# Optimization experiments

Hardware: AMD Instinct MI355X
Metric: run time of the kernel (lower is better)

## Reference

```python
import jax, jax.numpy as jnp
import numpy as np

IMG, P, INC = 384, 2, 3
C = 2 * IMG            # embed_dim = 768
NP_ = IMG // P         # 192 patches
N = NP_ + 1            # 193 tokens with cls
L, H, E, K, B = 6, 12, 8, 2, 32
HD = C // H
EPS = 1e-5


def layer_norm(x, w, b):
    m = jnp.mean(x, -1, keepdims=True)
    v = jnp.mean((x - m) ** 2, -1, keepdims=True)
    return (x - m) * jax.lax.rsqrt(v + EPS) * w + b


def setup_inputs() -> dict:
    key = jax.random.key(0)
    ks = iter(jax.random.split(key, 32))
    nrm = lambda sh, s=0.02: jax.random.normal(next(ks), sh, jnp.float32) * s
    inp = {
        'x1': nrm((B, INC, IMG, IMG), 1.0),
        'x2': nrm((B, INC, IMG, IMG), 1.0),
        'patch_w': nrm((C, INC, IMG, P)),
        'patch_b': jnp.zeros((C,)),
        'cls_token': nrm((1, 1, C), 1e-6),
        'ln1_w': jnp.ones((L, C)), 'ln1_b': jnp.zeros((L, C)),
        'qkv_w': nrm((L, 3 * C, C)), 'qkv_b': jnp.zeros((L, 3 * C)),
        'proj_w': nrm((L, C, C)), 'proj_b': jnp.zeros((L, C)),
        'ln2_w': jnp.ones((L, C)), 'ln2_b': jnp.zeros((L, C)),
        'route_w': nrm((L, E, C)), 'route_b': jnp.zeros((L, E)),
        'rln_w': jnp.ones((L, E)), 'rln_b': jnp.zeros((L, E)),
        'expert_w': nrm((L, E, C, C)), 'expert_b': jnp.zeros((L, E, C)),
        'norm_w': jnp.ones((C,)), 'norm_b': jnp.zeros((C,)),
    }
    # fixed 1D sin-cos positional embedding (build_sincos_encoding)
    pd = C // 2
    omega = jnp.exp(jnp.arange(pd, dtype=jnp.float32) * (-np.log(10000.0) / pd))
    ow = jnp.arange(NP_, dtype=jnp.float32)[:, None] * omega
    pe = jnp.concatenate([jnp.sin(ow), jnp.cos(ow)], axis=1)          # [192, C]
    inp['pos_emb'] = jnp.concatenate([jnp.zeros((1, C)), pe], axis=0)[None]  # [1, N, C]
    return inp


def _patch_embed(x, patch_w, patch_b, cls_token, pos_emb):
    b = x.shape[0]
    # non-overlapping (IMG, P) conv == matmul on patches, flattened in (c, kh, kw) order
    xp = x.reshape(b, INC, IMG, NP_, P).transpose(0, 3, 1, 2, 4).reshape(b, NP_, INC * IMG * P)
    tok = xp @ patch_w.reshape(C, -1).T + patch_b                     # [B, 192, C]
    tok = jnp.concatenate([jnp.broadcast_to(cls_token, (b, 1, C)), tok], axis=1)
    return tok + pos_emb


def _encoder(x, view_id, ln1_w, ln1_b, qkv_w, qkv_b, proj_w, proj_b,
             ln2_w, ln2_b, route_w, route_b, rln_w, rln_b, expert_w, expert_b):
    scale = HD ** -0.5
    base = jax.random.fold_in(jax.random.key(1234), view_id)
    b = x.shape[0]

    def step(h, p):
        idx, l1w, l1b, qw, qb, pw, pb, l2w, l2b, rw, rb, rlw, rlb, ew, eb = p
        # --- attention ---
        y = layer_norm(h, l1w, l1b)
        qkv = (y @ qw.T + qb).reshape(b, N, 3, H, HD).transpose(2, 0, 3, 1, 4)
        q, k, v = qkv[0], qkv[1], qkv[2]
        a = jax.nn.softmax(jnp.einsum('bhqd,bhkd->bhqk', q, k) * scale, axis=-1)
        o = jnp.einsum('bhqk,bhkd->bhqd', a, v).transpose(0, 2, 1, 3).reshape(b, N, C)
        h = h + o @ pw.T + pb
        # --- MoE ---
        y = layer_norm(h, l2w, l2b)
        logits = layer_norm(y @ rw.T + rb, rlw, rlb)                  # [B, N, E]
        noise = jax.random.normal(jax.random.fold_in(base, idx), logits.shape) / E
        rwts = jax.nn.softmax(logits, axis=-1) + noise
        topw, topi = jax.lax.top_k(rwts, K)
        topw = jax.nn.softmax(topw, axis=-1)
        # dense all-expert compute, as in the source module
        eo = jnp.einsum('bni,eoi->bneo', y, ew) + eb                  # [B, N, E, C]
        sel = jnp.take_along_axis(eo, topi[..., None], axis=2)        # [B, N, K, C]
        h = h + (sel * topw[..., None]).sum(axis=2)
        return h, None

    xs = (jnp.arange(L), ln1_w, ln1_b, qkv_w, qkv_b, proj_w, proj_b,
          ln2_w, ln2_b, route_w, route_b, rln_w, rln_b, expert_w, expert_b)
    x, _ = jax.lax.scan(step, x, xs)
    return x


def reference(x1, x2, patch_w, patch_b, cls_token, ln1_w, ln1_b, qkv_w, qkv_b,
              proj_w, proj_b, ln2_w, ln2_b, route_w, route_b, rln_w, rln_b,
              expert_w, expert_b, norm_w, norm_b, pos_emb):
    def tower(x, vid):
        h = _patch_embed(x, patch_w, patch_b, cls_token, pos_emb)
        h = _encoder(h, vid, ln1_w, ln1_b, qkv_w, qkv_b, proj_w, proj_b,
                     ln2_w, ln2_b, route_w, route_b, rln_w, rln_b, expert_w, expert_b)
        return layer_norm(h, norm_w, norm_b)[:, 0]
    return jnp.concatenate([tower(x1, 0), tower(x2, 1)], axis=1)      # [B, 2*C]
```

## Files before the change

kernel.cpp:

```cpp
#include <hip/hip_runtime.h>
#include <stdint.h>

#define C_DIM   768
#define N_TOK   193
#define B_TOT   64
#define ROWS    (B_TOT * N_TOK)
#define QKV_DIM 2304
#define N_HEAD  12
#define N_EXP   8
#define MAXPER  ROWS
#define RTOK    64

enum { MODE_PATCH = 0, MODE_PLAIN = 1, MODE_RESID = 2, MODE_EXPERT = 3 };

typedef __attribute__((ext_vector_type(8))) short bf16x8;
typedef __attribute__((ext_vector_type(4))) float f32x4;

__device__ __forceinline__ uint32_t rotl32(uint32_t x, int n){ return (x << n) | (x >> (32 - n)); }

__device__ __forceinline__ void tf2x32(uint32_t k0, uint32_t k1, uint32_t x0, uint32_t x1,
                                       uint32_t &r0, uint32_t &r1){
  uint32_t k2 = k0 ^ k1 ^ 0x1BD11BDAu;
#define TF4(a,b,c,d) x0+=x1; x1=rotl32(x1,a); x1^=x0; x0+=x1; x1=rotl32(x1,b); x1^=x0; \
                     x0+=x1; x1=rotl32(x1,c); x1^=x0; x0+=x1; x1=rotl32(x1,d); x1^=x0;
  x0 += k0; x1 += k1;
  TF4(13,15,26, 6)  x0 += k1; x1 += k2 + 1u;
  TF4(17,29,16,24)  x0 += k2; x1 += k0 + 2u;
  TF4(13,15,26, 6)  x0 += k0; x1 += k1 + 3u;
  TF4(17,29,16,24)  x0 += k1; x1 += k2 + 4u;
  TF4(13,15,26, 6)  x0 += k2; x1 += k0 + 5u;
#undef TF4
  r0 = x0; r1 = x1;
}

__device__ __forceinline__ float jax_erfinv(float x){
  float w = -log1pf(-x * x);
  float p;
  if (w < 5.0f){
    w -= 2.5f;
    p =              2.81022636e-08f;
    p = fmaf(p, w,   3.43273939e-07f);
    p = fmaf(p, w,  -3.5233877e-06f);
    p = fmaf(p, w,  -4.39150654e-06f);
    p = fmaf(p, w,   0.00021858087f);
    p = fmaf(p, w,  -0.00125372503f);
    p = fmaf(p, w,  -0.00417768164f);
    p = fmaf(p, w,   0.246640727f);
    p = fmaf(p, w,   1.50140941f);
  } else {
    w = sqrtf(w) - 3.0f;
    p =             -0.000200214257f;
    p = fmaf(p, w,   0.000100950558f);
    p = fmaf(p, w,   0.00134934322f);
    p = fmaf(p, w,  -0.00367342844f);
    p = fmaf(p, w,   0.00573950773f);
    p = fmaf(p, w,  -0.0076224613f);
    p = fmaf(p, w,   0.00943887047f);
    p = fmaf(p, w,   1.00167406f);
    p = fmaf(p, w,   2.83297682f);
  }
  return p * x;
}

__device__ __forceinline__ float jax_noise(uint32_t c0, uint32_t c1, uint32_t j){
  uint32_t o0, o1;
  tf2x32(c0, c1, 0u, j, o0, o1);
  uint32_t bits = o0 ^ o1;
  float f = __uint_as_float(0x3f800000u | (bits >> 9)) - 1.0f;
  const float lo = -0.99999994f;
  float u = fmaxf(lo, f * 2.0f + lo);
  return 1.41421356237f * jax_erfinv(u) * 0.125f;
}

__device__ __forceinline__ unsigned short f2bf(float x){
  union { float f; uint32_t u; } v; v.f = x;
  uint32_t u = v.u;
  uint32_t r = (u + 0x7FFFu + ((u >> 16) & 1u)) >> 16;
  return (unsigned short)r;
}
__device__ __forceinline__ float bf2f(unsigned short h){
  union { uint32_t u; float f; } v; v.u = ((uint32_t)h) << 16;
  return v.f;
}

__global__ __launch_bounds__(64) void k_zero8(int* __restrict__ p){
  if ((int)threadIdx.x < N_EXP) p[threadIdx.x] = 0;
}

__global__ __launch_bounds__(64) void k_sentinel(float* __restrict__ out, float v){
  if (threadIdx.x == 0) out[0] = v;
}

__global__ __launch_bounds__(256) void k_cls(float* __restrict__ h, const float* __restrict__ cls,
                                             const float* __restrict__ pos){
  const int bt = blockIdx.x;
  #pragma unroll
  for (int u = 0; u < 3; ++u){
    int c = threadIdx.x + u * 256;
    h[(size_t)bt * N_TOK * C_DIM + c] = cls[c] + pos[c];
  }
}

__device__ __forceinline__ float blk_sum(float v, float* sb){
  #pragma unroll
  for (int off = 32; off > 0; off >>= 1) v += __shfl_down(v, off, 64);
  const int lane = threadIdx.x & 63, w = threadIdx.x >> 6;
  if (lane == 0) sb[w] = v;
  __syncthreads();
  if (threadIdx.x == 0) sb[4] = sb[0] + sb[1] + sb[2] + sb[3];
  __syncthreads();
  float r = sb[4];
  __syncthreads();
  return r;
}

__global__ __launch_bounds__(256) void k_layernorm(const float* __restrict__ x, float* __restrict__ y,
                                                   const float* __restrict__ w, const float* __restrict__ b){
  __shared__ float sb[8];
  const float* xr = x + (size_t)blockIdx.x * C_DIM;
  float v0 = xr[threadIdx.x], v1 = xr[threadIdx.x + 256], v2 = xr[threadIdx.x + 512];
  float mean = blk_sum(v0 + v1 + v2, sb) * (1.0f / 768.0f);
  float d0 = v0 - mean, d1 = v1 - mean, d2 = v2 - mean;
  float var = blk_sum(d0 * d0 + d1 * d1 + d2 * d2, sb) * (1.0f / 768.0f);
  float inv = 1.0f / sqrtf(var + 1e-5f);
  float* yr = y + (size_t)blockIdx.x * C_DIM;
  yr[threadIdx.x]       = d0 * inv * w[threadIdx.x]       + b[threadIdx.x];
  yr[threadIdx.x + 256] = d1 * inv * w[threadIdx.x + 256] + b[threadIdx.x + 256];
  yr[threadIdx.x + 512] = d2 * inv * w[threadIdx.x + 512] + b[threadIdx.x + 512];
}

__global__ __launch_bounds__(256) void k_final(const float* __restrict__ h, float* __restrict__ out,
                                               const float* __restrict__ w, const float* __restrict__ b){
  __shared__ float sb[8];
  const int bt = blockIdx.x;
  const float* xr = h + (size_t)bt * N_TOK * C_DIM;
  float v0 = xr[threadIdx.x], v1 = xr[threadIdx.x + 256], v2 = xr[threadIdx.x + 512];
  float mean = blk_sum(v0 + v1 + v2, sb) * (1.0f / 768.0f);
  float d0 = v0 - mean, d1 = v1 - mean, d2 = v2 - mean;
  float var = blk_sum(d0 * d0 + d1 * d1 + d2 * d2, sb) * (1.0f / 768.0f);
  float inv = 1.0f / sqrtf(var + 1e-5f);
  float* orow = out + (size_t)(bt & 31) * 1536 + (size_t)(bt >> 5) * C_DIM;
  orow[threadIdx.x]       = d0 * inv * w[threadIdx.x]       + b[threadIdx.x];
  orow[threadIdx.x + 256] = d1 * inv * w[threadIdx.x + 256] + b[threadIdx.x + 256];
  orow[threadIdx.x + 512] = d2 * inv * w[threadIdx.x + 512] + b[threadIdx.x + 512];
}

template<int MODE>
__global__ __launch_bounds__(256) void k_mgemm(
    const float* __restrict__ A, const float* __restrict__ W,
    const float* __restrict__ bias, float* __restrict__ C,
    int M, int Nc, int Kc,
    const float* __restrict__ xa, const float* __restrict__ xb,
    const float* __restrict__ pos,
    const int* __restrict__ elist, const int* __restrict__ ecnt)
{
  __shared__ short sAhi[128][40];
  __shared__ short sAlo[128][40];
  __shared__ short sBhi[128][40];
  __shared__ short sBlo[128][40];

  const int tid = threadIdx.x;

  int e = 0;
  int Mloc = M;
  const float* Wp = W;
  const float* bp = bias;
  if constexpr (MODE == MODE_EXPERT){
    e = blockIdx.z;
    Mloc = ecnt[e];
    Wp = W + (size_t)e * C_DIM * C_DIM;
    bp = bias + e * C_DIM;
  }
  const int row0 = blockIdx.x * 128;
  const int col0 = blockIdx.y * 128;
  if (row0 >= Mloc) return;

  const int srow = tid >> 1;
  const int skh  = (tid & 1) * 16;

  const float* arow = A;
  bool avalid = false;
  const float* psrc = nullptr;
  if constexpr (MODE == MODE_PLAIN || MODE == MODE_RESID){
    int r = row0 + srow;
    avalid = r < Mloc;
    arow = A + (size_t)(avalid ? r : 0) * Kc;
  } else if constexpr (MODE == MODE_EXPERT){
    int r = row0 + srow;
    avalid = r < Mloc;
    if (avalid) arow = A + (size_t)(elist[e * MAXPER + r] >> 1) * C_DIM;
  } else {
    int r = row0 + srow;
    int bt = r / 192;
    int n  = r - bt * 192;
    const float* xp = (bt < 32) ? xa : xb;
    psrc = xp + (size_t)(bt & 31) * 3 * 384 * 384 + n * 2;
    avalid = true;
  }
  const float* brow = Wp + (size_t)(col0 + srow) * Kc;

  const int wv = tid >> 6;
  const int wr = (wv >> 1) * 64;
  const int wc = (wv & 1) * 64;
  const int lane = tid & 63;
  const int lrow = lane & 15;
  const int lkh  = (lane >> 4) * 8;

  f32x4 acc[4][4] = {};

  const int nkt = Kc / 32;
  for (int kt = 0; kt < nkt; ++kt){
    const int k0 = kt * 32 + skh;
    {
      float va[16] = {};
      if constexpr (MODE == MODE_PATCH){
        int c   = k0 / 768;
        int rem = k0 - c * 768;
        const float* pc = psrc + ((size_t)c * 384 + (rem >> 1)) * 384;
        #pragma unroll
        for (int m = 0; m < 8; ++m){
          va[m * 2 + 0] = pc[(size_t)m * 384 + 0];
          va[m * 2 + 1] = pc[(size_t)m * 384 + 1];
        }
      } else {
        if (avalid){
          *(float4*)&va[0]  = *(const float4*)(arow + k0);
          *(float4*)&va[4]  = *(const float4*)(arow + k0 + 4);
          *(float4*)&va[8]  = *(const float4*)(arow + k0 + 8);
          *(float4*)&va[12] = *(const float4*)(arow + k0 + 12);
        }
      }
      short hi[16], lo[16];
      #pragma unroll
      for (int j = 0; j < 16; ++j){
        unsigned short hb = f2bf(va[j]);
        hi[j] = (short)hb;
        lo[j] = (short)f2bf(va[j] - bf2f(hb));
      }
      *(bf16x8*)&sAhi[srow][skh]     = *(bf16x8*)&hi[0];
      *(bf16x8*)&sAhi[srow][skh + 8] = *(bf16x8*)&hi[8];
      *(bf16x8*)&sAlo[srow][skh]     = *(bf16x8*)&lo[0];
      *(bf16x8*)&sAlo[srow][skh + 8] = *(bf16x8*)&lo[8];
    }
    {
      float vb[16];
      *(float4*)&vb[0]  = *(const float4*)(brow + k0);
      *(float4*)&vb[4]  = *(const float4*)(brow + k0 + 4);
      *(float4*)&vb[8]  = *(const float4*)(brow + k0 + 8);
      *(float4*)&vb[12] = *(const float4*)(brow + k0 + 12);
      short hi[16], lo[16];
      #pragma unroll
      for (int j = 0; j < 16; ++j){
        unsigned short hb = f2bf(vb[j]);
        hi[j] = (short)hb;
        lo[j] = (short)f2bf(vb[j] - bf2f(hb));
      }
      *(bf16x8*)&sBhi[srow][skh]     = *(bf16x8*)&hi[0];
      *(bf16x8*)&sBhi[srow][skh + 8] = *(bf16x8*)&hi[8];
      *(bf16x8*)&sBlo[srow][skh]     = *(bf16x8*)&lo[0];
      *(bf16x8*)&sBlo[srow][skh + 8] = *(bf16x8*)&lo[8];
    }
    __syncthreads();
    bf16x8 ahi[4], alo[4], bhi[4], blo[4];
    #pragma unroll
    for (int i = 0; i < 4; ++i){
      ahi[i] = *(const bf16x8*)&sAhi[wr + i * 16 + lrow][lkh];
      alo[i] = *(const bf16x8*)&sAlo[wr + i * 16 + lrow][lkh];
    }
    #pragma unroll
    for (int j = 0; j < 4; ++j){
      bhi[j] = *(const bf16x8*)&sBhi[wc + j * 16 + lrow][lkh];
      blo[j] = *(const bf16x8*)&sBlo[wc + j * 16 + lrow][lkh];
    }
    #pragma unroll
    for (int i = 0; i < 4; ++i)
      #pragma unroll
      for (int j = 0; j < 4; ++j){
        acc[i][j] = __builtin_amdgcn_mfma_f32_16x16x32_bf16(ahi[i], bhi[j], acc[i][j], 0, 0, 0);
        acc[i][j] = __builtin_amdgcn_mfma_f32_16x16x32_bf16(ahi[i], blo[j], acc[i][j], 0, 0, 0);
        acc[i][j] = __builtin_amdgcn_mfma_f32_16x16x32_bf16(alo[i], bhi[j], acc[i][j], 0, 0, 0);
      }
    __syncthreads();
  }

  #pragma unroll
  for (int i = 0; i < 4; ++i){
    const int rbase = row0 + wr + i * 16 + (lane >> 4) * 4;
    #pragma unroll
    for (int r = 0; r < 4; ++r){
      const int rg = rbase + r;
      if (rg >= Mloc) continue;
      if constexpr (MODE == MODE_PATCH){
        int bt = rg / 192, n = rg - (rg / 192) * 192;
        size_t orow = ((size_t)bt * N_TOK + n + 1) * C_DIM;
        size_t prow = (size_t)(n + 1) * C_DIM;
        #pragma unroll
        for (int j = 0; j < 4; ++j){
          int cg = col0 + wc + j * 16 + (lane & 15);
          C[orow + cg] = acc[i][j][r] + bp[cg] + pos[prow + cg];
        }
      } else if constexpr (MODE == MODE_PLAIN){
        size_t orow = (size_t)rg * Nc;
        #pragma unroll
        for (int j = 0; j < 4; ++j){
          int cg = col0 + wc + j * 16 + (lane & 15);
          C[orow + cg] = acc[i][j][r] + bp[cg];
        }
      } else if constexpr (MODE == MODE_RESID){
        size_t orow = (size_t)rg * Nc;
        #pragma unroll
        for (int j = 0; j < 4; ++j){
          int cg = col0 + wc + j * 16 + (lane & 15);
          C[orow + cg] += acc[i][j][r] + bp[cg];
        }
      } else {
        int ts = elist[e * MAXPER + rg];
        size_t orow = (size_t)ts * C_DIM;
        #pragma unroll
        for (int j = 0; j < 4; ++j){
          int cg = col0 + wc + j * 16 + (lane & 15);
          C[orow + cg] = acc[i][j][r] + bp[cg];
        }
      }
    }
  }
}

__global__ __launch_bounds__(256) void k_attn(const float* __restrict__ qkv, float* __restrict__ o_out){
  __shared__ float Qs[64][64];
  __shared__ float KPs[64][64];
  __shared__ float Vs[64][64];
  const int q0 = blockIdx.x * 64;
  const int bh = blockIdx.y;
  const int bt = bh / N_HEAD, hh = bh - bt * N_HEAD;
  const int tid = threadIdx.x;
  const int tx = tid & 15, ty = tid >> 4;
  const size_t base = (size_t)bt * N_TOK * QKV_DIM + (size_t)hh * 64;

  {
    int m = tid & 63, g = tid >> 6;
    int q = q0 + m;
    bool valid = q < N_TOK;
    const float* src = qkv + base + (size_t)(valid ? q : 0) * QKV_DIM;
    #pragma unroll
    for (int u = 0; u < 4; ++u){
      int cb = (g * 4 + u) * 4;
      float4 v = valid ? *(const float4*)(src + cb) : make_float4(0.f,0.f,0.f,0.f);
      Qs[cb + 0][m] = v.x; Qs[cb + 1][m] = v.y; Qs[cb + 2][m] = v.z; Qs[cb + 3][m] = v.w;
    }
  }

  float Oa[4][4] = {};
  float mrun[4] = {-1e30f, -1e30f, -1e30f, -1e30f};
  float lrun[4] = {};

  for (int kt = 0; kt < 4; ++kt){
    const int n0 = kt * 64;
    __syncthreads();
    {
      int m = tid & 63, g = tid >> 6;
      int kk = n0 + m;
      bool valid = kk < N_TOK;
      const float* src = qkv + base + 768 + (size_t)(valid ? kk : 0) * QKV_DIM;
      #pragma unroll
      for (int u = 0; u < 4; ++u){
        int cb = (g * 4 + u) * 4;
        float4 v = valid ? *(const float4*)(src + cb) : make_float4(0.f,0.f,0.f,0.f);
        KPs[cb + 0][m] = v.x; KPs[cb + 1][m] = v.y; KPs[cb + 2][m] = v.z; KPs[cb + 3][m] = v.w;
      }
    }
    {
      int c4 = tid & 15, nr = tid >> 4;
      #pragma unroll
      for (int r = 0; r < 4; ++r){
        int n = nr + r * 16;
        int kk = n0 + n;
        float4 v = (kk < N_TOK) ? *(const float4*)(qkv + base + 1536 + (size_t)kk * QKV_DIM + c4 * 4)
                                : make_float4(0.f,0.f,0.f,0.f);
        *(float4*)&Vs[n][c4 * 4] = v;
      }
    }
    __syncthreads();
    float s[4][4] = {};
    #pragma unroll 8
    for (int d = 0; d < 64; ++d){
      float4 a4 = *(const float4*)&Qs[d][ty * 4];
      float4 b4 = *(const float4*)&KPs[d][tx * 4];
      float av[4] = {a4.x, a4.y, a4.z, a4.w};
      float bv[4] = {b4.x, b4.y, b4.z, b4.w};
      #pragma unroll
      for (int i = 0; i < 4; ++i)
        #pragma unroll
        for (int j = 0; j < 4; ++j)
          s[i][j] = fmaf(av[i], bv[j], s[i][j]);
    }
    #pragma unroll
    for (int i = 0; i < 4; ++i)
      #pragma unroll
      for (int j = 0; j < 4; ++j){
        s[i][j] *= 0.125f;
        if (n0 + tx * 4 + j >= N_TOK) s[i][j] = -1e30f;
      }
    __syncthreads();
    #pragma unroll
    for (int i = 0; i < 4; ++i){
      float rm = fmaxf(fmaxf(s[i][0], s[i][1]), fmaxf(s[i][2], s[i][3]));
      rm = fmaxf(rm, __shfl_xor(rm, 1, 64));
      rm = fmaxf(rm, __shfl_xor(rm, 2, 64));
      rm = fmaxf(rm, __shfl_xor(rm, 4, 64));
      rm = fmaxf(rm, __shfl_xor(rm, 8, 64));
      float mn = fmaxf(mrun[i], rm);
      float fac = expf(mrun[i] - mn);
      mrun[i] = mn;
      lrun[i] *= fac;
      float p[4], rs = 0.f;
      #pragma unroll
      for (int j = 0; j < 4; ++j){ p[j] = expf(s[i][j] - mn); rs += p[j]; }
      rs += __shfl_xor(rs, 1, 64);
      rs += __shfl_xor(rs, 2, 64);
      rs += __shfl_xor(rs, 4, 64);
      rs += __shfl_xor(rs, 8, 64);
      lrun[i] += rs;
      #pragma unroll
      for (int j = 0; j < 4; ++j){ Oa[i][j] *= fac; KPs[ty * 4 + i][tx * 4 + j] = p[j]; }
    }
    __syncthreads();
    #pragma unroll 4
    for (int n = 0; n < 64; ++n){
      float4 v4 = *(const float4*)&Vs[n][tx * 4];
      float vv[4] = {v4.x, v4.y, v4.z, v4.w};
      #pragma unroll
      for (int i = 0; i < 4; ++i){
        float pv = KPs[ty * 4 + i][n];
        #pragma unroll
        for (int j = 0; j < 4; ++j)
          Oa[i][j] = fmaf(pv, vv[j], Oa[i][j]);
      }
    }
  }
  #pragma unroll
  for (int i = 0; i < 4; ++i){
    int q = q0 + ty * 4 + i;
    if (q < N_TOK){
      float inv = 1.0f / lrun[i];
      #pragma unroll
      for (int j = 0; j < 4; ++j)
        o_out[((size_t)bt * N_TOK + q) * C_DIM + hh * 64 + tx * 4 + j] = Oa[i][j] * inv;
    }
  }
}

__global__ __launch_bounds__(256) void k_router(
    const float* __restrict__ y, const float* __restrict__ rw, const float* __restrict__ rb,
    const float* __restrict__ rlw, const float* __restrict__ rlb,
    float* __restrict__ topw, int* __restrict__ elist, int* __restrict__ ecnt, int l)
{
  __shared__ float4 sw4[1536];
  __shared__ int lcnt[8];
  __shared__ int lbase[8];
  __shared__ int llist[8][RTOK];
  const int tid = threadIdx.x;
  const float4* rw4 = (const float4*)rw;
  #pragma unroll
  for (int u = 0; u < 6; ++u)
    sw4[tid + u * 256] = rw4[tid + u * 256];
  if (tid < 8) lcnt[tid] = 0;
  __syncthreads();

  const int wid = tid >> 6, lane = tid & 63;
  const int e = lane & 7;

  for (int t16 = 0; t16 < RTOK / 4; ++t16){
    const int tok = blockIdx.x * RTOK + wid * (RTOK / 4) + t16;
    const float4* y4 = (const float4*)(y + (size_t)tok * C_DIM);
    const float4 a0 = y4[lane], a1 = y4[64 + lane], a2 = y4[128 + lane];

    float part[8];
    #pragma unroll
    for (int ee = 0; ee < 8; ++ee){
      const float4 w0 = sw4[ee * 192 + lane];
      const float4 w1 = sw4[ee * 192 + 64 + lane];
      const float4 w2 = sw4[ee * 192 + 128 + lane];
      float s = a0.x * w0.x;
      s = fmaf(a0.y, w0.y, s); s = fmaf(a0.z, w0.z, s); s = fmaf(a0.w, w0.w, s);
      s = fmaf(a1.x, w1.x, s); s = fmaf(a1.y, w1.y, s); s = fmaf(a1.z, w1.z, s); s = fmaf(a1.w, w1.w, s);
      s = fmaf(a2.x, w2.x, s); s = fmaf(a2.y, w2.y, s); s = fmaf(a2.z, w2.z, s); s = fmaf(a2.w, w2.w, s);
      part[ee] = s;
    }
    #pragma unroll
    for (int ee = 0; ee < 8; ++ee)
      #pragma unroll
      for (int off = 32; off; off >>= 1) part[ee] += __shfl_xor(part[ee], off, 64);

    float logit = part[e] + rb[e];
    float ssum = logit;
    ssum += __shfl_xor(ssum, 1, 64); ssum += __shfl_xor(ssum, 2, 64); ssum += __shfl_xor(ssum, 4, 64);
    float mean = ssum * 0.125f;
    float d = logit - mean;
    float vs = d * d;
    vs += __shfl_xor(vs, 1, 64); vs += __shfl_xor(vs, 2, 64); vs += __shfl_xor(vs, 4, 64);
    float ln = d * (1.0f / sqrtf(vs * 0.125f + 1e-5f)) * rlw[e] + rlb[e];
    float mx = ln;
    mx = fmaxf(mx, __shfl_xor(mx, 1, 64)); mx = fmaxf(mx, __shfl_xor(mx, 2, 64)); mx = fmaxf(mx, __shfl_xor(mx, 4, 64));
    float ex = expf(ln - mx);
    float es = ex;
    es += __shfl_xor(es, 1, 64); es += __shfl_xor(es, 2, 64); es += __shfl_xor(es, 4, 64);
    float prob = ex / es;
    int t = tok / 6176;
    int rem = tok - t * 6176;
    int b = rem / N_TOK, n = rem - (rem / N_TOK) * N_TOK;
    uint32_t b0, b1, c0, c1;
    tf2x32(0u, 1234u, 0u, (uint32_t)t, b0, b1);
    tf2x32(b0, b1, 0u, (uint32_t)l, c0, c1);
    uint32_t j = (uint32_t)(b * N_TOK + n) * 8u + (uint32_t)e;
    float r = prob + jax_noise(c0, c1, j);
    float v1 = r; int i1 = e;
    #pragma unroll
    for (int off = 1; off <= 4; off <<= 1){
      float ov = __shfl_xor(v1, off, 64); int oi = __shfl_xor(i1, off, 64);
      if (ov > v1 || (ov == v1 && oi < i1)){ v1 = ov; i1 = oi; }
    }
    float rm2 = (e == i1) ? -3.0e38f : r;
    float v2 = rm2; int i2 = e;
    #pragma unroll
    for (int off = 1; off <= 4; off <<= 1){
      float ov = __shfl_xor(v2, off, 64); int oi = __shfl_xor(i2, off, 64);
      if (ov > v2 || (ov == v2 && oi < i2)){ v2 = ov; i2 = oi; }
    }
    float e2 = expf(v2 - v1);
    float sum = 1.0f + e2;
    if (lane == 0){
      topw[tok * 2 + 0] = 1.0f / sum;
      topw[tok * 2 + 1] = e2 / sum;
      int p = atomicAdd(&lcnt[i1], 1);
      llist[i1][p] = tok * 2;
      int p2 = atomicAdd(&lcnt[i2], 1);
      llist[i2][p2] = tok * 2 + 1;
    }
  }
  __syncthreads();
  if (tid < 8) lbase[tid] = atomicAdd(&ecnt[tid], lcnt[tid]);
  __syncthreads();
  #pragma unroll
  for (int ee = 0; ee < 8; ++ee){
    const int cnt = lcnt[ee];
    const int bse = lbase[ee];
    for (int i = tid; i < cnt; i += 256)
      elist[ee * MAXPER + bse + i] = llist[ee][i];
  }
}

__global__ __launch_bounds__(256) void k_combine(float* __restrict__ h, const float* __restrict__ eout,
                                                 const float* __restrict__ topw){
  const int tok = blockIdx.x;
  const float w0 = topw[tok * 2], w1 = topw[tok * 2 + 1];
  const size_t hb = (size_t)tok * C_DIM;
  const size_t e0 = (size_t)(tok * 2) * C_DIM, e1 = e0 + C_DIM;
  #pragma unroll
  for (int u = 0; u < 3; ++u){
    int c = threadIdx.x + u * 256;
    h[hb + c] += w0 * eout[e0 + c] + w1 * eout[e1 + c];
  }
}

extern "C" void kernel_launch(void* const* d_in, const int* in_sizes, int n_in,
                              void* d_out, int out_size, void* d_ws, size_t ws_size,
                              hipStream_t stream){
  float* out = (float*)d_out;

  static const int kExp[22] = {
    14155776, 14155776, 1769472, 768, 768,
    4608, 4608, 10616832, 13824, 3538944, 4608,
    4608, 4608, 36864, 48, 48, 48,
    28311552, 36864, 768, 768, 148224};
  const size_t need_f = (size_t)ROWS * C_DIM * 2 + (size_t)ROWS * QKV_DIM
                      + (size_t)ROWS * 2 + (size_t)N_EXP * MAXPER + 8;
  float bad = 0.f;
  if (n_in != 22) bad = 2.0e6f;
  else {
    for (int i = 0; i < 22; ++i)
      if (in_sizes[i] != kExp[i]){ bad = 4.0e6f + i * 1.0e4f; break; }
  }
  if (bad == 0.f && out_size != 49152) bad = 3.0e6f;
  if (bad == 0.f && ws_size < need_f * 4) bad = 1.0e6f;
  if (bad != 0.f){
    k_sentinel<<<dim3(1), 64, 0, stream>>>(out, bad);
    return;
  }

  const float* x1       = (const float*)d_in[0];
  const float* x2       = (const float*)d_in[1];
  const float* patch_w  = (const float*)d_in[2];
  const float* patch_b  = (const float*)d_in[3];
  const float* cls_tok  = (const float*)d_in[4];
  const float* ln1_w    = (const float*)d_in[5];
  const float* ln1_b    = (const float*)d_in[6];
  const float* qkv_w    = (const float*)d_in[7];
  const float* qkv_b    = (const float*)d_in[8];
  const float* proj_w   = (const float*)d_in[9];
  const float* proj_b   = (const float*)d_in[10];
  const float* ln2_w    = (const float*)d_in[11];
  const float* ln2_b    = (const float*)d_in[12];
  const float* route_w  = (const float*)d_in[13];
  const float* route_b  = (const float*)d_in[14];
  const float* rln_w    = (const float*)d_in[15];
  const float* rln_b    = (const float*)d_in[16];
  const float* expert_w = (const float*)d_in[17];
  const float* expert_b = (const float*)d_in[18];
  const float* norm_w   = (const float*)d_in[19];
  const float* norm_b   = (const float*)d_in[20];
  const float* pos_emb  = (const float*)d_in[21];

  float* ws = (float*)d_ws;
  size_t off = 0;
  float* h    = ws + off; off += (size_t)ROWS * C_DIM;
  float* y    = ws + off; off += (size_t)ROWS * C_DIM;
  float* qkv  = ws + off; off += (size_t)ROWS * QKV_DIM;
  float* eout = qkv;
  float* topw = ws + off; off += (size_t)ROWS * 2;
  int*   elist = (int*)(ws + off); off += (size_t)N_EXP * MAXPER;
  int*   ecnt  = (int*)(ws + off); off += 8;

  k_cls<<<dim3(B_TOT), 256, 0, stream>>>(h, cls_tok, pos_emb);
  k_mgemm<MODE_PATCH><<<dim3(96, 6), 256, 0, stream>>>(
      nullptr, patch_w, patch_b, h, 12288, C_DIM, 2304, x1, x2, pos_emb, nullptr, nullptr);

  for (int l = 0; l < 6; ++l){
    k_layernorm<<<dim3(ROWS), 256, 0, stream>>>(h, y, ln1_w + l * C_DIM, ln1_b + l * C_DIM);
    k_mgemm<MODE_PLAIN><<<dim3(97, 18), 256, 0, stream>>>(
        y, qkv_w + (size_t)l * QKV_DIM * C_DIM, qkv_b + l * QKV_DIM, qkv,
        ROWS, QKV_DIM, C_DIM, nullptr, nullptr, nullptr, nullptr, nullptr);
    k_attn<<<dim3(4, B_TOT * N_HEAD), 256, 0, stream>>>(qkv, y);
    k_mgemm<MODE_RESID><<<dim3(97, 6), 256, 0, stream>>>(
        y, proj_w + (size_t)l * C_DIM * C_DIM, proj_b + l * C_DIM, h,
        ROWS, C_DIM, C_DIM, nullptr, nullptr, nullptr, nullptr, nullptr);
    k_layernorm<<<dim3(ROWS), 256, 0, stream>>>(h, y, ln2_w + l * C_DIM, ln2_b + l * C_DIM);
    k_zero8<<<dim3(1), 64, 0, stream>>>(ecnt);
    k_router<<<dim3(ROWS / RTOK), 256, 0, stream>>>(
        y, route_w + (size_t)l * N_EXP * C_DIM, route_b + l * N_EXP,
        rln_w + l * N_EXP, rln_b + l * N_EXP, topw, elist, ecnt, l);
    k_mgemm<MODE_EXPERT><<<dim3(97, 6, N_EXP), 256, 0, stream>>>(
        y, expert_w + (size_t)l * N_EXP * C_DIM * C_DIM, expert_b + (size_t)l * N_EXP * C_DIM, eout,
        ROWS, C_DIM, C_DIM, nullptr, nullptr, nullptr, elist, ecnt);
    k_combine<<<dim3(ROWS), 256, 0, stream>>>(h, eout, topw);
  }
  k_final<<<dim3(B_TOT), 256, 0, stream>>>(h, out, norm_w, norm_b);
}
```

Before: 4.505 ms.

## Move attention QK^T and PV onto bf16 MFMA with hi/lo split precision

Rewrites the attention kernel to compute both the score matrix and the P·V product with 16x16x32 bf16 MFMA instructions instead of scalar FP32 FMAs. Each FP32 operand is split into bf16 hi and lo parts and three MFMAs per product recover near-FP32 accuracy. Shared-memory tiles are stored as padded bf16 arrays, with V transposed, and the softmax is rearranged to match the MFMA output layout. This adds conversion work and 3x MFMA count to reduce the FP32 ALU cost of attention, which is only one part of the whole model.

New measurement: 4.072 ms. 1.11x faster.

```diff
diff --git a/kernel.cpp b/kernel.cpp
--- a/kernel.cpp
+++ b/kernel.cpp
@@ -327,30 +327,48 @@
 }
 
 __global__ __launch_bounds__(256) void k_attn(const float* __restrict__ qkv, float* __restrict__ o_out){
-  __shared__ float Qs[64][64];
-  __shared__ float KPs[64][64];
-  __shared__ float Vs[64][64];
+  __shared__ short sQhi[64][72],  sQlo[64][72];
+  __shared__ short sKPhi[64][72], sKPlo[64][72];
+  __shared__ short sVThi[64][72], sVTlo[64][72];
+
   const int q0 = blockIdx.x * 64;
   const int bh = blockIdx.y;
   const int bt = bh / N_HEAD, hh = bh - bt * N_HEAD;
   const int tid = threadIdx.x;
-  const int tx = tid & 15, ty = tid >> 4;
   const size_t base = (size_t)bt * N_TOK * QKV_DIM + (size_t)hh * 64;
 
+  const int srow = tid >> 2;
+  const int sk   = (tid & 3) * 16;
+
   {
-    int m = tid & 63, g = tid >> 6;
-    int q = q0 + m;
-    bool valid = q < N_TOK;
-    const float* src = qkv + base + (size_t)(valid ? q : 0) * QKV_DIM;
-    #pragma unroll
-    for (int u = 0; u < 4; ++u){
-      int cb = (g * 4 + u) * 4;
-      float4 v = valid ? *(const float4*)(src + cb) : make_float4(0.f,0.f,0.f,0.f);
-      Qs[cb + 0][m] = v.x; Qs[cb + 1][m] = v.y; Qs[cb + 2][m] = v.z; Qs[cb + 3][m] = v.w;
-    }
-  }
-
-  float Oa[4][4] = {};
+    float v[16] = {};
+    int q = q0 + srow;
+    if (q < N_TOK){
+      const float* src = qkv + base + (size_t)q * QKV_DIM + sk;
+      *(float4*)&v[0]  = *(const float4*)(src);
+      *(float4*)&v[4]  = *(const float4*)(src + 4);
+      *(float4*)&v[8]  = *(const float4*)(src + 8);
+      *(float4*)&v[12] = *(const float4*)(src + 12);
+    }
+    short hi[16], lo[16];
+    #pragma unroll
+    for (int j = 0; j < 16; ++j){
+      unsigned short hb = f2bf(v[j]);
+      hi[j] = (short)hb;
+      lo[j] = (short)f2bf(v[j] - bf2f(hb));
+    }
+    *(bf16x8*)&sQhi[srow][sk]     = *(bf16x8*)&hi[0];
+    *(bf16x8*)&sQhi[srow][sk + 8] = *(bf16x8*)&hi[8];
+    *(bf16x8*)&sQlo[srow][sk]     = *(bf16x8*)&lo[0];
+    *(bf16x8*)&sQlo[srow][sk + 8] = *(bf16x8*)&lo[8];
+  }
+
+  const int wv   = tid >> 6;
+  const int lane = tid & 63;
+  const int lrow = lane & 15;
+  const int lkh  = (lane >> 4) * 8;
+
+  f32x4 Oacc[4] = {};
   float mrun[4] = {-1e30f, -1e30f, -1e30f, -1e30f};
   float lrun[4] = {};
 
@@ -358,94 +376,139 @@
     const int n0 = kt * 64;
     __syncthreads();
     {
-      int m = tid & 63, g = tid >> 6;
-      int kk = n0 + m;
+      float v[16] = {};
+      int kk = n0 + srow;
       bool valid = kk < N_TOK;
-      const float* src = qkv + base + 768 + (size_t)(valid ? kk : 0) * QKV_DIM;
-      #pragma unroll
-      for (int u = 0; u < 4; ++u){
-        int cb = (g * 4 + u) * 4;
-        float4 v = valid ? *(const float4*)(src + cb) : make_float4(0.f,0.f,0.f,0.f);
-        KPs[cb + 0][m] = v.x; KPs[cb + 1][m] = v.y; KPs[cb + 2][m] = v.z; KPs[cb + 3][m] = v.w;
-      }
-    }
+      if (valid){
+        const float* src = qkv + base + 768 + (size_t)kk * QKV_DIM + sk;
+        *(float4*)&v[0]  = *(const float4*)(src);
+        *(float4*)&v[4]  = *(const float4*)(src + 4);
+        *(float4*)&v[8]  = *(const float4*)(src + 8);
+        *(float4*)&v[12] = *(const float4*)(src + 12);
+      }
+      short hi[16], lo[16];
+      #pragma unroll
+      for (int j = 0; j < 16; ++j){
+        unsigned short hb = f2bf(v[j]);
+        hi[j] = (short)hb;
+        lo[j] = (short)f2bf(v[j] - bf2f(hb));
+      }
+      *(bf16x8*)&sKPhi[srow][sk]     = *(bf16x8*)&hi[0];
+      *(bf16x8*)&sKPhi[srow][sk + 8] = *(bf16x8*)&hi[8];
+      *(bf16x8*)&sKPlo[srow][sk]     = *(bf16x8*)&lo[0];
+      *(bf16x8*)&sKPlo[srow][sk + 8] = *(bf16x8*)&lo[8];
+      float vv[16] = {};
+      if (valid){
+        const float* src = qkv + base + 1536 + (size_t)kk * QKV_DIM + sk;
+        *(float4*)&vv[0]  = *(const float4*)(src);
+        *(float4*)&vv[4]  = *(const float4*)(src + 4);
+        *(float4*)&vv[8]  = *(const float4*)(src + 8);
+        *(float4*)&vv[12] = *(const float4*)(src + 12);
+      }
+      #pragma unroll
+      for (int j = 0; j < 16; ++j){
+        unsigned short hb = f2bf(vv[j]);
+        sVThi[sk + j][srow] = (short)hb;
+        sVTlo[sk + j][srow] = (short)f2bf(vv[j] - bf2f(hb));
+      }
+    }
+    __syncthreads();
+
+    f32x4 s[4] = {};
     {
-      int c4 = tid & 15, nr = tid >> 4;
+      bf16x8 ahi0 = *(const bf16x8*)&sQhi[wv * 16 + lrow][lkh];
+      bf16x8 alo0 = *(const bf16x8*)&sQlo[wv * 16 + lrow][lkh];
+      bf16x8 ahi1 = *(const bf16x8*)&sQhi[wv * 16 + lrow][32 + lkh];
+      bf16x8 alo1 = *(const bf16x8*)&sQlo[wv * 16 + lrow][32 + lkh];
+      #pragma unroll
+      for (int j = 0; j < 4; ++j){
+        bf16x8 bhi0 = *(const bf16x8*)&sKPhi[j * 16 + lrow][lkh];
+        bf16x8 blo0 = *(const bf16x8*)&sKPlo[j * 16 + lrow][lkh];
+        bf16x8 bhi1 = *(const bf16x8*)&sKPhi[j * 16 + lrow][32 + lkh];
+        bf16x8 blo1 = *(const bf16x8*)&sKPlo[j * 16 + lrow][32 + lkh];
+        s[j] = __builtin_amdgcn_mfma_f32_16x16x32_bf16(ahi0, bhi0, s[j], 0, 0, 0);
+        s[j] = __builtin_amdgcn_mfma_f32_16x16x32_bf16(ahi0, blo0, s[j], 0, 0, 0);
+        s[j] = __builtin_amdgcn_mfma_f32_16x16x32_bf16(alo0, bhi0, s[j], 0, 0, 0);
+        s[j] = __builtin_amdgcn_mfma_f32_16x16x32_bf16(ahi1, bhi1, s[j], 0, 0, 0);
+        s[j] = __builtin_amdgcn_mfma_f32_16x16x32_bf16(ahi1, blo1, s[j], 0, 0, 0);
+        s[j] = __builtin_amdgcn_mfma_f32_16x16x32_bf16(alo1, bhi1, s[j], 0, 0, 0);
+      }
+    }
+    #pragma unroll
+    for (int j = 0; j < 4; ++j){
+      bool masked = (n0 + j * 16 + lrow) >= N_TOK;
       #pragma unroll
       for (int r = 0; r < 4; ++r){
-        int n = nr + r * 16;
-        int kk = n0 + n;
-        float4 v = (kk < N_TOK) ? *(const float4*)(qkv + base + 1536 + (size_t)kk * QKV_DIM + c4 * 4)
-                                : make_float4(0.f,0.f,0.f,0.f);
-        *(float4*)&Vs[n][c4 * 4] = v;
-      }
-    }
-    __syncthreads();
-    float s[4][4] = {};
-    #pragma unroll 8
-    for (int d = 0; d < 64; ++d){
-      float4 a4 = *(const float4*)&Qs[d][ty * 4];
-      float4 b4 = *(const float4*)&KPs[d][tx * 4];
-      float av[4] = {a4.x, a4.y, a4.z, a4.w};
-      float bv[4] = {b4.x, b4.y, b4.z, b4.w};
-      #pragma unroll
-      for (int i = 0; i < 4; ++i)
-        #pragma unroll
-        for (int j = 0; j < 4; ++j)
-          s[i][j] = fmaf(av[i], bv[j], s[i][j]);
-    }
-    #pragma unroll
-    for (int i = 0; i < 4; ++i)
-      #pragma unroll
-      for (int j = 0; j < 4; ++j){
-        s[i][j] *= 0.125f;
-        if (n0 + tx * 4 + j >= N_TOK) s[i][j] = -1e30f;
-      }
-    __syncthreads();
-    #pragma unroll
-    for (int i = 0; i < 4; ++i){
-      float rm = fmaxf(fmaxf(s[i][0], s[i][1]), fmaxf(s[i][2], s[i][3]));
+        s[j][r] *= 0.125f;
+        if (masked) s[j][r] = -1e30f;
+      }
+    }
+
+    float p[4][4], fac[4];
+    #pragma unroll
+    for (int r = 0; r < 4; ++r){
+      float rm = fmaxf(fmaxf(s[0][r], s[1][r]), fmaxf(s[2][r], s[3][r]));
       rm = fmaxf(rm, __shfl_xor(rm, 1, 64));
       rm = fmaxf(rm, __shfl_xor(rm, 2, 64));
       rm = fmaxf(rm, __shfl_xor(rm, 4, 64));
       rm = fmaxf(rm, __shfl_xor(rm, 8, 64));
-      float mn = fmaxf(mrun[i], rm);
-      float fac = expf(mrun[i] - mn);
-      mrun[i] = mn;
-      lrun[i] *= fac;
-      float p[4], rs = 0.f;
-      #pragma unroll
-      for (int j = 0; j < 4; ++j){ p[j] = expf(s[i][j] - mn); rs += p[j]; }
+      float mn = fmaxf(mrun[r], rm);
+      fac[r] = expf(mrun[r] - mn);
+      mrun[r] = mn;
+      lrun[r] *= fac[r];
+      float rs = 0.f;
+      #pragma unroll
+      for (int j = 0; j < 4; ++j){ p[j][r] = expf(s[j][r] - mn); rs += p[j][r]; }
       rs += __shfl_xor(rs, 1, 64);
       rs += __shfl_xor(rs, 2, 64);
       rs += __shfl_xor(rs, 4, 64);
       rs += __shfl_xor(rs, 8, 64);
-      lrun[i] += rs;
-      #pragma unroll
-      for (int j = 0; j < 4; ++j){ Oa[i][j] *= fac; KPs[ty * 4 + i][tx * 4 + j] = p[j]; }
-    }
+      lrun[r] += rs;
+      #pragma unroll
+      for (int j = 0; j < 4; ++j) Oacc[j][r] *= fac[r];
+    }
+
     __syncthreads();
-    #pragma unroll 4
-    for (int n = 0; n < 64; ++n){
-      float4 v4 = *(const float4*)&Vs[n][tx * 4];
-      float vv[4] = {v4.x, v4.y, v4.z, v4.w};
-      #pragma unroll
-      for (int i = 0; i < 4; ++i){
-        float pv = KPs[ty * 4 + i][n];
-        #pragma unroll
-        for (int j = 0; j < 4; ++j)
-          Oa[i][j] = fmaf(pv, vv[j], Oa[i][j]);
-      }
-    }
-  }
+    #pragma unroll
+    for (int r = 0; r < 4; ++r){
+      const int prow = wv * 16 + (lane >> 4) * 4 + r;
+      #pragma unroll
+      for (int j = 0; j < 4; ++j){
+        unsigned short hb = f2bf(p[j][r]);
+        sKPhi[prow][j * 16 + lrow] = (short)hb;
+        sKPlo[prow][j * 16 + lrow] = (short)f2bf(p[j][r] - bf2f(hb));
+      }
+    }
+
+    {
+      bf16x8 phi0 = *(const bf16x8*)&sKPhi[wv * 16 + lrow][lkh];
+      bf16x8 plo0 = *(const bf16x8*)&sKPlo[wv * 16 + lrow][lkh];
+      bf16x8 phi1 = *(const bf16x8*)&sKPhi[wv * 16 + lrow][32 + lkh];
+      bf16x8 plo1 = *(const bf16x8*)&sKPlo[wv * 16 + lrow][32 + lkh];
+      #pragma unroll
+      for (int j = 0; j < 4; ++j){
+        bf16x8 vhi0 = *(const bf16x8*)&sVThi[j * 16 + lrow][lkh];
+        bf16x8 vlo0 = *(const bf16x8*)&sVTlo[j * 16 + lrow][lkh];
+        bf16x8 vhi1 = *(const bf16x8*)&sVThi[j * 16 + lrow][32 + lkh];
+        bf16x8 vlo1 = *(const bf16x8*)&sVTlo[j * 16 + lrow][32 + lkh];
+        Oacc[j] = __builtin_amdgcn_mfma_f32_16x16x32_bf16(phi0, vhi0, Oacc[j], 0, 0, 0);
+        Oacc[j] = __builtin_amdgcn_mfma_f32_16x16x32_bf16(phi0, vlo0, Oacc[j], 0, 0, 0);
+        Oacc[j] = __builtin_amdgcn_mfma_f32_16x16x32_bf16(plo0, vhi0, Oacc[j], 0, 0, 0);
+        Oacc[j] = __builtin_amdgcn_mfma_f32_16x16x32_bf16(phi1, vhi1, Oacc[j], 0, 0, 0);
+        Oacc[j] = __builtin_amdgcn_mfma_f32_16x16x32_bf16(phi1, vlo1, Oacc[j], 0, 0, 0);
+        Oacc[j] = __builtin_amdgcn_mfma_f32_16x16x32_bf16(plo1, vhi1, Oacc[j], 0, 0, 0);
+      }
+    }
+  }
+
   #pragma unroll
-  for (int i = 0; i < 4; ++i){
-    int q = q0 + ty * 4 + i;
+  for (int r = 0; r < 4; ++r){
+    int q = q0 + wv * 16 + (lane >> 4) * 4 + r;
     if (q < N_TOK){
-      float inv = 1.0f / lrun[i];
+      float inv = 1.0f / lrun[r];
       #pragma unroll
       for (int j = 0; j < 4; ++j)
-        o_out[((size_t)bt * N_TOK + q) * C_DIM + hh * 64 + tx * 4 + j] = Oa[i][j] * inv;
+        o_out[((size_t)bt * N_TOK + q) * C_DIM + hh * 64 + j * 16 + lrow] = Oacc[j][r] * inv;
     }
   }
 }
```
